# Kernel tuning notes

Hardware: AMD Instinct MI355X
Metric: run time of the kernel (lower is better)

## Reference

```python
import jax, jax.numpy as jnp
import numpy as np

N = 50000
E = 1600000
IN_DIM = 1433
TOPO_HIDDEN = 64
ALIGN_DIM = 32
NUM_CLASSES = 7


def setup_inputs() -> dict:
    key = jax.random.key(0)
    ks = jax.random.split(key, 10)
    x = jax.random.normal(ks[0], (N, IN_DIM), dtype=jnp.float32)
    edge_index = jax.random.randint(ks[1], (2, E), 0, N, dtype=jnp.int64)

    def glorot(k, fan_in, fan_out):
        lim = float(np.sqrt(6.0 / (fan_in + fan_out)))
        return jax.random.uniform(k, (fan_in, fan_out), jnp.float32, -lim, lim)

    return {
        "x": x,
        "edge_index": edge_index,
        "W_gcn": glorot(ks[2], IN_DIM, TOPO_HIDDEN),
        "b_gcn": jnp.zeros((TOPO_HIDDEN,), jnp.float32),
        "W_pt": glorot(ks[3], TOPO_HIDDEN, ALIGN_DIM),
        "b_pt": jnp.zeros((ALIGN_DIM,), jnp.float32),
        "W_ps": glorot(ks[4], IN_DIM, ALIGN_DIM),
        "b_ps": jnp.zeros((ALIGN_DIM,), jnp.float32),
        "W_cls": glorot(ks[5], ALIGN_DIM, NUM_CLASSES),
        "b_cls": jnp.zeros((NUM_CLASSES,), jnp.float32),
    }


def gcn_conv(x, edge_index, W, b, num_nodes):
    """PyG GCNConv: linear transform, then sym-normalized aggregation with self-loops."""
    src, dst = edge_index[0], edge_index[1]
    loop = jnp.arange(num_nodes, dtype=src.dtype)
    src = jnp.concatenate([src, loop])  # [E+N]
    dst = jnp.concatenate([dst, loop])

    xw = x @ W  # [N, H]

    deg = jax.ops.segment_sum(jnp.ones_like(dst, dtype=xw.dtype), dst,
                              num_segments=num_nodes)  # [N], >=1 due to self-loops
    dis = jax.lax.rsqrt(deg)
    norm = dis[src] * dis[dst]  # [E+N]

    msgs = xw[src] * norm[:, None]  # [E+N, H]
    out = jax.ops.segment_sum(msgs, dst, num_segments=num_nodes)
    return out + b


def reference(x, edge_index, W_gcn, b_gcn, W_pt, b_pt, W_ps, b_ps, W_cls, b_cls):
    h_topo = jax.nn.relu(gcn_conv(x, edge_index, W_gcn, b_gcn, x.shape[0]))
    z_topo = h_topo @ W_pt + b_pt  # [N, align_dim]
    z_sem = x @ W_ps + b_ps        # [N, align_dim]
    logits = z_topo @ W_cls + b_cls  # [N, num_classes]
    diff = z_topo - z_sem
    anomaly_scores = jnp.sqrt(jnp.sum(diff * diff, axis=-1))  # L2 norm per node
    return (logits, anomaly_scores, z_topo, z_sem)
```

## Files before the change

kernel.cpp:

```cpp
#include <hip/hip_runtime.h>
#include <math.h>

#define IN_DIM 1433
#define KPAD 1472
#define H_TOPO 64
#define ALIGN 32
#define NCLS 7
#define NT 23
#define CAP 128

typedef __attribute__((ext_vector_type(8))) short short8;
typedef __attribute__((ext_vector_type(4))) short short4v;
typedef __attribute__((ext_vector_type(4))) float floatx4;
typedef __attribute__((ext_vector_type(4))) unsigned int uint4v;
typedef float float4u __attribute__((ext_vector_type(4), aligned(4)));

__device__ inline unsigned short f2bf(float f) {
    union { float f; unsigned u; } v; v.f = f;
    unsigned r = v.u + 0x7FFF + ((v.u >> 16) & 1);
    return (unsigned short)(r >> 16);
}


__global__ void k_prep(const float* __restrict__ Wg, const float* __restrict__ Wp,
                       unsigned short* __restrict__ wT, int* __restrict__ cursor, int n) {
    int i = blockIdx.x * blockDim.x + threadIdx.x;
    if (i < n) cursor[i] = 0;
    if (i < 96 * KPAD) {
        int c = i / KPAD, k = i - c * KPAD;
        float v = 0.0f;
        if (k < IN_DIM) v = (c < 64) ? Wg[k * 64 + c] : Wp[k * 32 + (c - 64)];
        wT[i] = f2bf(v);
    }
}


__global__ void k_fill(const int* __restrict__ ei, int* __restrict__ cursor,
                       int* __restrict__ col, int E) {
    int e = blockIdx.x * blockDim.x + threadIdx.x;
    if (e >= E) return;
    int dst = ei[E + e];
    int pos = atomicAdd(&cursor[dst], 1) & (CAP - 1);
    col[dst * CAP + pos] = ei[e];
}


#define BM 128
#define BK 64
#define APAD 72

__global__ __launch_bounds__(256) void k_gemm(
    const float* __restrict__ x, const unsigned short* __restrict__ wT,
    const float* __restrict__ bps, const int* __restrict__ deg,
    unsigned short* __restrict__ xwsb, float* __restrict__ zsem, int n)
{
    __shared__ unsigned short a_lds[BM * APAD];
    __shared__ unsigned short b_lds[96 * APAD];

    int t = threadIdx.x;
    int row0 = blockIdx.x * BM;
    int w  = t >> 6;
    int l  = t & 63;
    int lm = l & 15;
    int lg = l >> 4;
    int c4 = t & 15;
    int rb = t >> 4;

    floatx4 acc[2][6] = {};
    float4u aPf[8];
    short8  bPf[3];

    auto load_tile = [&](int k0) {
        if (k0 + BK <= IN_DIM) {
            #pragma unroll
            for (int p = 0; p < 8; ++p) {
                int gr = row0 + p * 16 + rb;
                float4u v = {};
                if (gr < n) v = *(const float4u*)&x[(long)gr * IN_DIM + k0 + 4 * c4];
                aPf[p] = v;
            }
        } else {
            #pragma unroll
            for (int p = 0; p < 8; ++p) {
                int gr = row0 + p * 16 + rb;
                float4u v = {};
                if (gr < n) {
                    #pragma unroll
                    for (int q = 0; q < 4; ++q) {
                        int gk = k0 + 4 * c4 + q;
                        v[q] = (gk < IN_DIM) ? x[(long)gr * IN_DIM + gk] : 0.0f;
                    }
                }
                aPf[p] = v;
            }
        }
        #pragma unroll
        for (int it = 0; it < 3; ++it) {
            int idx = it * 256 + t;
            int c = idx >> 3, kc = (idx & 7) * 8;
            bPf[it] = *(const short8*)&wT[c * KPAD + k0 + kc];
        }
    };
    auto store_tile = [&]() {
        #pragma unroll
        for (int p = 0; p < 8; ++p) {
            short4v pv;
            pv.x = (short)f2bf(aPf[p].x); pv.y = (short)f2bf(aPf[p].y);
            pv.z = (short)f2bf(aPf[p].z); pv.w = (short)f2bf(aPf[p].w);
            *(short4v*)&a_lds[(p * 16 + rb) * APAD + 4 * c4] = pv;
        }
        #pragma unroll
        for (int it = 0; it < 3; ++it) {
            int idx = it * 256 + t;
            int c = idx >> 3, kc = (idx & 7) * 8;
            *(short8*)&b_lds[c * APAD + kc] = bPf[it];
        }
    };

    load_tile(0);
    store_tile();
    __syncthreads();

    for (int kt = 0; kt < NT; ++kt) {
        if (kt + 1 < NT) load_tile((kt + 1) * BK);
        #pragma unroll
        for (int h = 0; h < 2; ++h) {
            int koff = h * 32 + lg * 8;
            short8 a0 = *(const short8*)&a_lds[(w * 32 + lm) * APAD + koff];
            short8 a1 = *(const short8*)&a_lds[(w * 32 + 16 + lm) * APAD + koff];
            #pragma unroll
            for (int j = 0; j < 6; ++j) {
                short8 bf = *(const short8*)&b_lds[(j * 16 + lm) * APAD + koff];
                acc[0][j] = __builtin_amdgcn_mfma_f32_16x16x32_bf16(a0, bf, acc[0][j], 0, 0, 0);
                acc[1][j] = __builtin_amdgcn_mfma_f32_16x16x32_bf16(a1, bf, acc[1][j], 0, 0, 0);
            }
        }
        __syncthreads();
        if (kt + 1 < NT) {
            store_tile();
            __syncthreads();
        }
    }

    #pragma unroll
    for (int mt = 0; mt < 2; ++mt) {
        #pragma unroll
        for (int r = 0; r < 4; ++r) {
            int grow = row0 + w * 32 + mt * 16 + lg * 4 + r;
            if (grow >= n) continue;
            float d = rsqrtf(1.0f + (float)deg[grow]);
            #pragma unroll
            for (int j = 0; j < 6; ++j) {
                int c = j * 16 + lm;
                float v = acc[mt][j][r];
                if (c < 64) {
                    xwsb[(long)grow * 64 + c] = f2bf(v * d);
                } else {
                    zsem[(long)grow * 32 + (c - 64)] = v + bps[c - 64];
                }
            }
        }
    }
}


__global__ __launch_bounds__(256) void k_pullhead(
    const int* __restrict__ deg, const int* __restrict__ col,
    const unsigned short* __restrict__ xwsb,
    const float* __restrict__ bgcn, const float* __restrict__ Wpt,
    const float* __restrict__ bpt, const float* __restrict__ Wcls,
    const float* __restrict__ bcls, const float* __restrict__ zsem,
    float* __restrict__ logits, float* __restrict__ anom,
    float* __restrict__ ztopo, int n)
{
    __shared__ float sW[H_TOPO * ALIGN];
    __shared__ float sC[ALIGN * NCLS];
    __shared__ float sbp[ALIGN], sbc[NCLS], sbg[H_TOPO];
    __shared__ float hrow[4][H_TOPO];
    __shared__ float zrow[4][ALIGN];

    int t = threadIdx.x;
    for (int i = t; i < H_TOPO * ALIGN; i += 256) sW[i] = Wpt[i];
    for (int i = t; i < ALIGN * NCLS; i += 256) sC[i] = Wcls[i];
    if (t < ALIGN) sbp[t] = bpt[t];
    if (t < NCLS) sbc[t] = bcls[t];
    if (t < H_TOPO) sbg[t] = bgcn[t];

    int w    = t >> 6;
    int lane = t & 63;
    int ng = lane >> 3;
    int f8 = lane & 7;
    int dst = blockIdx.x * 4 + w;
    bool active = dst < n;

    __syncthreads();

    float acc[8] = {};
    int c0 = 0;
    if (active) {
        c0 = deg[dst];
        int c = (c0 > CAP) ? CAP : c0;
        int s = dst * CAP;
        for (int j0 = 0; j0 < c; j0 += 64) {
            int m = c - j0; if (m > 64) m = 64;
            int idx = (lane < m) ? col[s + j0 + lane] : -1;
            for (int j = 0; j < m; j += 8) {
                int sj = __shfl(idx, j + ng);
                if (sj >= 0) {
                    uint4v v = *(const uint4v*)&xwsb[(long)sj * 64 + f8 * 8];
                    #pragma unroll
                    for (int q = 0; q < 4; ++q) {
                        acc[2 * q]     += __uint_as_float(v[q] << 16);
                        acc[2 * q + 1] += __uint_as_float(v[q] & 0xffff0000u);
                    }
                }
            }
        }
    }
    #pragma unroll
    for (int q = 0; q < 8; ++q) {
        acc[q] += __shfl_xor(acc[q], 8);
        acc[q] += __shfl_xor(acc[q], 16);
        acc[q] += __shfl_xor(acc[q], 32);
    }

    if (active && ng == 0) {
        float dd = rsqrtf(1.0f + (float)c0);
        uint4v v = *(const uint4v*)&xwsb[(long)dst * 64 + f8 * 8];
        #pragma unroll
        for (int q = 0; q < 4; ++q) {
            float s0 = __uint_as_float(v[q] << 16);
            float s1 = __uint_as_float(v[q] & 0xffff0000u);
            int k0 = f8 * 8 + 2 * q;
            hrow[w][k0]     = fmaxf((acc[2 * q]     + s0) * dd + sbg[k0],     0.0f);
            hrow[w][k0 + 1] = fmaxf((acc[2 * q + 1] + s1) * dd + sbg[k0 + 1], 0.0f);
        }
    }
    __syncthreads();

    int j = lane & 31;
    float z = sbp[j];
    #pragma unroll 8
    for (int k = 0; k < H_TOPO; ++k) z += hrow[w][k] * sW[k * ALIGN + j];

    if (active && lane < 32) {
        ztopo[(long)dst * ALIGN + j] = z;
        zrow[w][j] = z;
    }

    float zs = active ? zsem[(long)dst * ALIGN + j] : 0.0f;
    float d = z - zs;
    float ss = d * d;
    ss += __shfl_xor(ss, 1);
    ss += __shfl_xor(ss, 2);
    ss += __shfl_xor(ss, 4);
    ss += __shfl_xor(ss, 8);
    ss += __shfl_xor(ss, 16);
    if (active && lane == 0) anom[dst] = sqrtf(ss);

    __syncthreads();

    if (active && lane < NCLS) {
        float lg = sbc[lane];
        #pragma unroll
        for (int jj = 0; jj < ALIGN; ++jj) lg += zrow[w][jj] * sC[jj * NCLS + lane];
        logits[(long)dst * NCLS + lane] = lg;
    }
}


extern "C" void kernel_launch(void* const* d_in, const int* in_sizes, int n_in,
                              void* d_out, int out_size, void* d_ws, size_t ws_size,
                              hipStream_t stream) {
    const float* x   = (const float*)d_in[0];
    const int*   ei  = (const int*)d_in[1];
    const float* Wg  = (const float*)d_in[2];
    const float* bg  = (const float*)d_in[3];
    const float* Wpt = (const float*)d_in[4];
    const float* bpt = (const float*)d_in[5];
    const float* Wps = (const float*)d_in[6];
    const float* bps = (const float*)d_in[7];
    const float* Wc  = (const float*)d_in[8];
    const float* bc  = (const float*)d_in[9];

    int n = in_sizes[0] / IN_DIM;
    int E = in_sizes[1] / 2;

    float* out    = (float*)d_out;
    float* logits = out;
    float* anom   = logits + (long)n * NCLS;
    float* ztopo  = anom + n;
    float* zsem   = ztopo + (long)n * ALIGN;

    int* cursor = (int*)d_ws;
    int* col    = cursor + n;
    unsigned short* wT   = (unsigned short*)(col + (long)n * CAP);
    unsigned short* xwsb = wT + 96 * KPAD;

    k_prep  <<<(96 * KPAD + 255) / 256, 256, 0, stream>>>(Wg, Wps, wT, cursor, n);
    k_fill  <<<(E + 255) / 256, 256, 0, stream>>>(ei, cursor, col, E);
    k_gemm  <<<(n + BM - 1) / BM, 256, 0, stream>>>(x, wT, bps, cursor, xwsb, zsem, n);
    k_pullhead <<<(n + 3) / 4, 256, 0, stream>>>(cursor, col, xwsb,
                                                 bg, Wpt, bpt, Wc, bc, zsem,
                                                 logits, anom, ztopo, n);
}
```

Measured before the change: 597.8 us.

## Fuse edge fill into GEMM launch and move source degree scaling to pull

```diff
diff --git a/kernel.cpp b/kernel.cpp
--- a/kernel.cpp
+++ b/kernel.cpp
@@ -35,30 +35,33 @@
 }
 
 
-__global__ void k_fill(const int* __restrict__ ei, int* __restrict__ cursor,
-                       int* __restrict__ col, int E) {
-    int e = blockIdx.x * blockDim.x + threadIdx.x;
-    if (e >= E) return;
-    int dst = ei[E + e];
-    int pos = atomicAdd(&cursor[dst], 1) & (CAP - 1);
-    col[dst * CAP + pos] = ei[e];
-}
-
-
 #define BM 128
 #define BK 64
 #define APAD 72
 
-__global__ __launch_bounds__(256) void k_gemm(
+__global__ __launch_bounds__(256) void k_gemmfill(
     const float* __restrict__ x, const unsigned short* __restrict__ wT,
-    const float* __restrict__ bps, const int* __restrict__ deg,
-    unsigned short* __restrict__ xwsb, float* __restrict__ zsem, int n)
+    const float* __restrict__ bps,
+    unsigned short* __restrict__ xwsb, float* __restrict__ zsem, int n,
+    const int* __restrict__ ei, int* __restrict__ cursor, int* __restrict__ col,
+    int E, int ngemm)
 {
     __shared__ unsigned short a_lds[BM * APAD];
     __shared__ unsigned short b_lds[96 * APAD];
 
+    int bid = blockIdx.x;
+    if (bid >= ngemm) {
+        int e = (bid - ngemm) * 256 + threadIdx.x;
+        if (e < E) {
+            int dst = ei[E + e];
+            int pos = atomicAdd(&cursor[dst], 1) & (CAP - 1);
+            col[dst * CAP + pos] = ei[e];
+        }
+        return;
+    }
+
     int t = threadIdx.x;
-    int row0 = blockIdx.x * BM;
+    int row0 = bid * BM;
     int w  = t >> 6;
     int l  = t & 63;
     int lm = l & 15;
@@ -148,13 +151,12 @@
         for (int r = 0; r < 4; ++r) {
             int grow = row0 + w * 32 + mt * 16 + lg * 4 + r;
             if (grow >= n) continue;
-            float d = rsqrtf(1.0f + (float)deg[grow]);
             #pragma unroll
             for (int j = 0; j < 6; ++j) {
                 int c = j * 16 + lm;
                 float v = acc[mt][j][r];
                 if (c < 64) {
-                    xwsb[(long)grow * 64 + c] = f2bf(v * d);
+                    xwsb[(long)grow * 64 + c] = f2bf(v);
                 } else {
                     zsem[(long)grow * 32 + (c - 64)] = v + bps[c - 64];
                 }
@@ -203,15 +205,21 @@
         int s = dst * CAP;
         for (int j0 = 0; j0 < c; j0 += 64) {
             int m = c - j0; if (m > 64) m = 64;
-            int idx = (lane < m) ? col[s + j0 + lane] : -1;
+            int idx = -1;
+            float disv = 0.0f;
+            if (lane < m) {
+                idx = col[s + j0 + lane];
+                disv = rsqrtf(1.0f + (float)deg[idx]);
+            }
             for (int j = 0; j < m; j += 8) {
                 int sj = __shfl(idx, j + ng);
+                float sdis = __shfl(disv, j + ng);
                 if (sj >= 0) {
                     uint4v v = *(const uint4v*)&xwsb[(long)sj * 64 + f8 * 8];
                     #pragma unroll
                     for (int q = 0; q < 4; ++q) {
-                        acc[2 * q]     += __uint_as_float(v[q] << 16);
-                        acc[2 * q + 1] += __uint_as_float(v[q] & 0xffff0000u);
+                        acc[2 * q]     = fmaf(__uint_as_float(v[q] << 16),          sdis, acc[2 * q]);
+                        acc[2 * q + 1] = fmaf(__uint_as_float(v[q] & 0xffff0000u), sdis, acc[2 * q + 1]);
                     }
                 }
             }
@@ -229,8 +237,8 @@
         uint4v v = *(const uint4v*)&xwsb[(long)dst * 64 + f8 * 8];
         #pragma unroll
         for (int q = 0; q < 4; ++q) {
-            float s0 = __uint_as_float(v[q] << 16);
-            float s1 = __uint_as_float(v[q] & 0xffff0000u);
+            float s0 = __uint_as_float(v[q] << 16)          * dd;
+            float s1 = __uint_as_float(v[q] & 0xffff0000u)  * dd;
             int k0 = f8 * 8 + 2 * q;
             hrow[w][k0]     = fmaxf((acc[2 * q]     + s0) * dd + sbg[k0],     0.0f);
             hrow[w][k0 + 1] = fmaxf((acc[2 * q + 1] + s1) * dd + sbg[k0 + 1], 0.0f);
@@ -297,9 +305,12 @@
     unsigned short* wT   = (unsigned short*)(col + (long)n * CAP);
     unsigned short* xwsb = wT + 96 * KPAD;
 
+    int ngemm = (n + BM - 1) / BM;
+    int nfill = (E + 255) / 256;
+
     k_prep  <<<(96 * KPAD + 255) / 256, 256, 0, stream>>>(Wg, Wps, wT, cursor, n);
-    k_fill  <<<(E + 255) / 256, 256, 0, stream>>>(ei, cursor, col, E);
-    k_gemm  <<<(n + BM - 1) / BM, 256, 0, stream>>>(x, wT, bps, cursor, xwsb, zsem, n);
+    k_gemmfill <<<ngemm + nfill, 256, 0, stream>>>(x, wT, bps, xwsb, zsem, n,
+                                                   ei, cursor, col, E, ngemm);
     k_pullhead <<<(n + 3) / 4, 256, 0, stream>>>(cursor, col, xwsb,
                                                  bg, Wpt, bpt, Wc, bc, zsem,
                                                  logits, anom, ztopo, n);
```

Result: faster. 560.0 us (-6.3%).
